# Kernel tuning notes

Hardware: AMD Instinct MI355X
Metric: run time of the kernel (lower is better)

The kernel has to match this reference:

```python
import jax, jax.numpy as jnp
import numpy as np

M, N, L = 1024, 1024, 64  # spatial rows, spatial cols, spectral bands


def setup_inputs() -> dict:
    key = jax.random.key(0)
    k1, k2 = jax.random.split(key)
    x = jax.random.uniform(k1, (1, M, N, L), dtype=jnp.float32)   # spectral cube
    ca = jax.random.uniform(k2, (1, M, N, 1), dtype=jnp.float32)  # coded aperture
    return {"x": x, "ca": ca}


def reference(x, ca):
    """CASSI forward: y[m, n+l] += x[m, n, l] * ca[m, n].

    Faithful to forward_cassi's loop of L pad+add ops, but expressed as a
    single vectorized scatter-add along the dispersion diagonal.
    """
    _, m, n, l = x.shape
    y1 = (x * ca)[0]                                       # (M, N, L) coded cube
    # destination column for band l at column n is n + l
    idx = jnp.arange(n)[:, None] + jnp.arange(l)[None, :]  # (N, L)
    y2 = jnp.zeros((m, n + l - 1), dtype=x.dtype).at[:, idx].add(y1)
    return y2[None, :, :, None]                            # (1, M, N+L-1, 1)
```

## Files before the change

### kernel.cpp

```cpp
#include <hip/hip_runtime.h>


#define CASSI_M 1024
#define CASSI_N 1024
#define CASSI_L 64
#define CASSI_OUTW (CASSI_N + CASSI_L - 1)

constexpr int CN = 128;
constexpr int P = CASSI_L + 1;
constexpr int NCHUNK = CASSI_N / CN;
constexpr int BLK = 512;
constexpr int SPC = (CN * CASSI_L) / (BLK * 4);
constexpr int OWIN = CN + CASSI_L - 1;

__global__ __launch_bounds__(BLK) void cassi_chunk_kernel(
    const float* __restrict__ x, const float* __restrict__ ca,
    float* __restrict__ out) {
    __shared__ float xs[CN * P];

    const int bid = blockIdx.x;
    const int m = bid >> 3;
    const int c = bid & (NCHUNK - 1);
    const int n0 = c * CN;
    const int t = threadIdx.x;

    const float* __restrict__ xsrc = x + ((size_t)m * CASSI_N + n0) * CASSI_L;
    const float* __restrict__ csrc = ca + (size_t)m * CASSI_N + n0;

#pragma unroll
    for (int s = 0; s < SPC; ++s) {
        const int f = (s * BLK + t) * 4;
        const int nrel = f >> 6;
        const int l = f & 63;
        const float4 v = *reinterpret_cast<const float4*>(xsrc + f);
        const float cv = csrc[nrel];
        float* dst = &xs[nrel * P + l];
        dst[0] = v.x * cv;
        dst[1] = v.y * cv;
        dst[2] = v.z * cv;
        dst[3] = v.w * cv;
    }
    __syncthreads();

    if (t < OWIN) {
        const int k = t;
        float s0 = 0.0f, s1 = 0.0f;
#pragma unroll
        for (int l = 0; l < CASSI_L; l += 2) {
            const int n_a = k - l;
            const int n_b = k - l - 1;
            const float va = xs[(n_a & (CN - 1)) * P + l];
            const float vb = xs[(n_b & (CN - 1)) * P + l + 1];
            s0 += ((unsigned)n_a < (unsigned)CN) ? va : 0.0f;
            s1 += ((unsigned)n_b < (unsigned)CN) ? vb : 0.0f;
        }
        unsafeAtomicAdd(&out[(size_t)m * CASSI_OUTW + n0 + k], s0 + s1);
    }
}

extern "C" void kernel_launch(void* const* d_in, const int* in_sizes, int n_in,
                              void* d_out, int out_size, void* d_ws, size_t ws_size,
                              hipStream_t stream) {
    const float* x  = (const float*)d_in[0];
    const float* ca = (const float*)d_in[1];
    float* out = (float*)d_out;
    (void)in_sizes; (void)n_in; (void)d_ws; (void)ws_size;

    hipMemsetAsync(d_out, 0, (size_t)out_size * sizeof(float), stream);
    cassi_chunk_kernel<<<CASSI_M * NCHUNK, BLK, 0, stream>>>(x, ca, out);
}
```

Measured before the change: 359.4 us.

## Process full rows per block with shared-memory carry instead of atomics

Each block now walks all column chunks of one spatial row sequentially, passing the overlapping 63-column tail of each chunk to the next via a double-buffered shared carry array. This removes the output memset and the global atomic adds. In exchange the grid shrinks eightfold and chunks are processed serially with extra barriers, reducing memory-level parallelism.

New measurement: 359.0 us. Within noise of the previous version (-0.1%).

```diff
diff --git a/kernel.cpp b/kernel.cpp
--- a/kernel.cpp
+++ b/kernel.cpp
@@ -13,48 +13,69 @@
 constexpr int SPC = (CN * CASSI_L) / (BLK * 4);
 constexpr int OWIN = CN + CASSI_L - 1;
 
-__global__ __launch_bounds__(BLK) void cassi_chunk_kernel(
+__global__ __launch_bounds__(BLK) void cassi_row_kernel(
     const float* __restrict__ x, const float* __restrict__ ca,
     float* __restrict__ out) {
     __shared__ float xs[CN * P];
+    __shared__ float carry[2][CASSI_L];
 
-    const int bid = blockIdx.x;
-    const int m = bid >> 3;
-    const int c = bid & (NCHUNK - 1);
-    const int n0 = c * CN;
+    const int m = blockIdx.x;
     const int t = threadIdx.x;
 
-    const float* __restrict__ xsrc = x + ((size_t)m * CASSI_N + n0) * CASSI_L;
-    const float* __restrict__ csrc = ca + (size_t)m * CASSI_N + n0;
+    if (t < CASSI_L) {
+        carry[0][t] = 0.0f;
+        carry[1][t] = 0.0f;
+    }
+
+    const float* __restrict__ xrow = x + (size_t)m * CASSI_N * CASSI_L;
+    const float* __restrict__ crow = ca + (size_t)m * CASSI_N;
+    float* __restrict__ orow = out + (size_t)m * CASSI_OUTW;
+
+    for (int c = 0; c < NCHUNK; ++c) {
+        const int n0 = c * CN;
+        const float* __restrict__ xsrc = xrow + (size_t)n0 * CASSI_L;
+        const float* __restrict__ csrc = crow + n0;
 
 #pragma unroll
-    for (int s = 0; s < SPC; ++s) {
-        const int f = (s * BLK + t) * 4;
-        const int nrel = f >> 6;
-        const int l = f & 63;
-        const float4 v = *reinterpret_cast<const float4*>(xsrc + f);
-        const float cv = csrc[nrel];
-        float* dst = &xs[nrel * P + l];
-        dst[0] = v.x * cv;
-        dst[1] = v.y * cv;
-        dst[2] = v.z * cv;
-        dst[3] = v.w * cv;
-    }
-    __syncthreads();
+        for (int s = 0; s < SPC; ++s) {
+            const int f = (s * BLK + t) * 4;
+            const int nrel = f >> 6;
+            const int l = f & 63;
+            const float4 v = *reinterpret_cast<const float4*>(xsrc + f);
+            const float cv = csrc[nrel];
+            float* dst = &xs[nrel * P + l];
+            dst[0] = v.x * cv;
+            dst[1] = v.y * cv;
+            dst[2] = v.z * cv;
+            dst[3] = v.w * cv;
+        }
+        __syncthreads();
 
-    if (t < OWIN) {
-        const int k = t;
-        float s0 = 0.0f, s1 = 0.0f;
+        if (t < OWIN) {
+            const int k = t;
+            float s0 = 0.0f, s1 = 0.0f;
 #pragma unroll
-        for (int l = 0; l < CASSI_L; l += 2) {
-            const int n_a = k - l;
-            const int n_b = k - l - 1;
-            const float va = xs[(n_a & (CN - 1)) * P + l];
-            const float vb = xs[(n_b & (CN - 1)) * P + l + 1];
-            s0 += ((unsigned)n_a < (unsigned)CN) ? va : 0.0f;
-            s1 += ((unsigned)n_b < (unsigned)CN) ? vb : 0.0f;
+            for (int l = 0; l < CASSI_L; l += 2) {
+                const int n_a = k - l;
+                const int n_b = k - l - 1;
+                const float va = xs[(n_a & (CN - 1)) * P + l];
+                const float vb = xs[(n_b & (CN - 1)) * P + l + 1];
+                s0 += ((unsigned)n_a < (unsigned)CN) ? va : 0.0f;
+                s1 += ((unsigned)n_b < (unsigned)CN) ? vb : 0.0f;
+            }
+            const float s = s0 + s1;
+            const int cur = c & 1;
+            if (k < CASSI_L - 1) {
+                orow[n0 + k] = s + carry[cur][k];
+            } else if (k < CN) {
+                orow[n0 + k] = s;
+            } else if (c == NCHUNK - 1) {
+                orow[n0 + k] = s;
+            } else {
+                carry[cur ^ 1][k - CN] = s;
+            }
         }
-        unsafeAtomicAdd(&out[(size_t)m * CASSI_OUTW + n0 + k], s0 + s1);
+        __syncthreads();
     }
 }
 
@@ -64,8 +85,7 @@
     const float* x  = (const float*)d_in[0];
     const float* ca = (const float*)d_in[1];
     float* out = (float*)d_out;
-    (void)in_sizes; (void)n_in; (void)d_ws; (void)ws_size;
+    (void)in_sizes; (void)n_in; (void)d_ws; (void)ws_size; (void)out_size;
 
-    hipMemsetAsync(d_out, 0, (size_t)out_size * sizeof(float), stream);
-    cassi_chunk_kernel<<<CASSI_M * NCHUNK, BLK, 0, stream>>>(x, ca, out);
+    cassi_row_kernel<<<CASSI_M, BLK, 0, stream>>>(x, ca, out);
 }
```
